# Optimization experiments

Measured on AMD Instinct MI355X. Metric: run time of the kernel, lower is better.

## Reference

```python
import jax, jax.numpy as jnp
import numpy as np

EMBED_DIM = 768
NUM_HEADS = 12
HEAD_DIM = EMBED_DIM // NUM_HEADS  # 64
SCALE = HEAD_DIM ** 0.5  # NOTE: source MULTIPLIES by sqrt(head_dim) (likely a bug, kept faithful)


def setup_inputs() -> dict:
    key = jax.random.key(0)
    kx, kq, kk, kv, ko = jax.random.split(key, 5)
    B, N, E = 8, 2048, EMBED_DIM
    s = 1.0 / np.sqrt(E)
    return {
        "x": jax.random.normal(kx, (B, N, E), dtype=jnp.float32),
        # nn.Linear weights stored [out_features, in_features], y = x @ W.T
        "Wq": jax.random.normal(kq, (E, E), dtype=jnp.float32) * s,
        "Wk": jax.random.normal(kk, (E, E), dtype=jnp.float32) * s,
        "Wv": jax.random.normal(kv, (E, E), dtype=jnp.float32) * s,
        "Wo": jax.random.normal(ko, (E, E), dtype=jnp.float32) * s,
    }


def reference(x, Wq, Wk, Wv, Wo):
    # Projections (no bias)
    q = jnp.einsum("bne,fe->bnf", x, Wq)
    k = jnp.einsum("bne,fe->bnf", x, Wk)
    v = jnp.einsum("bne,fe->bnf", x, Wv)
    # Full-width attention over the entire embedding dim (no head split, per source)
    energy = jnp.einsum("bid,bjd->bij", q, k) * SCALE  # [B, N, N]
    attn = jax.nn.softmax(energy, axis=-1)
    out = jnp.einsum("bij,bjd->bid", attn, v)  # [B, N, E]
    return jnp.einsum("bne,fe->bnf", out, Wo)
```

## Files before the change

kernel.cpp:

```cpp
#include <hip/hip_runtime.h>
#include <stdint.h>

typedef __bf16 bf16;
typedef __bf16 bf16x4 __attribute__((ext_vector_type(4)));
typedef __bf16 bf16x8 __attribute__((ext_vector_type(8)));
typedef float  f32x4  __attribute__((ext_vector_type(4)));

constexpr int BB = 8;
constexpr int NN = 2048;
constexpr int EE = 768;
constexpr int MM = BB * NN;

typedef const __attribute__((address_space(1))) void* as1_cvp;
typedef __attribute__((address_space(3))) void* as3_vp;

static __device__ __forceinline__ void gld16(const void* g, void* l) {
  __builtin_amdgcn_global_load_lds((as1_cvp)g, (as3_vp)l, 16, 0, 0);
}

__global__ __launch_bounds__(256) void k_splitx(const float4* __restrict__ x,
                                                bf16x4* __restrict__ hi,
                                                bf16x4* __restrict__ lo, int n4) {
  int i = blockIdx.x * 256 + threadIdx.x;
  int st = gridDim.x * 256;
  for (; i < n4; i += st) {
    float4 v = x[i];
    bf16x4 h, l;
    h[0] = (bf16)v.x; l[0] = (bf16)(v.x - (float)h[0]);
    h[1] = (bf16)v.y; l[1] = (bf16)(v.y - (float)h[1]);
    h[2] = (bf16)v.z; l[2] = (bf16)(v.z - (float)h[2]);
    h[3] = (bf16)v.w; l[3] = (bf16)(v.w - (float)h[3]);
    hi[i] = h; lo[i] = l;
  }
}

__global__ __launch_bounds__(256) void k_cvt(const float4* __restrict__ src,
                                             bf16x4* __restrict__ dst, int n4) {
  int i = blockIdx.x * 256 + threadIdx.x;
  int st = gridDim.x * 256;
  for (; i < n4; i += st) {
    float4 v = src[i];
    bf16x4 h;
    h[0] = (bf16)v.x; h[1] = (bf16)v.y; h[2] = (bf16)v.z; h[3] = (bf16)v.w;
    dst[i] = h;
  }
}

template <bool PAIR>
__global__ __launch_bounds__(256) void k_wtrans(const float* __restrict__ src,
                                                bf16* __restrict__ hi,
                                                bf16* __restrict__ lo) {
  __shared__ float t[64][65];
  int e0 = blockIdx.x * 64, f0 = blockIdx.y * 64;
  int tid = threadIdx.x;
#pragma unroll
  for (int h = 0; h < 4; h++) {
    int lin = h * 1024 + tid * 4;
    int r = lin >> 6, c = lin & 63;
    float4 v = *(const float4*)(src + (size_t)(f0 + r) * EE + e0 + c);
    t[r][c] = v.x; t[r][c + 1] = v.y; t[r][c + 2] = v.z; t[r][c + 3] = v.w;
  }
  __syncthreads();
#pragma unroll
  for (int h = 0; h < 4; h++) {
    int lin = h * 1024 + tid * 4;
    int er = lin >> 6, fc = lin & 63;
    bf16x4 oh, ol;
#pragma unroll
    for (int j = 0; j < 4; j++) {
      float v = t[fc + j][er];
      bf16 hh = (bf16)v;
      oh[j] = hh;
      if constexpr (PAIR) ol[j] = (bf16)(v - (float)hh);
    }
    *(bf16x4*)(hi + (size_t)(e0 + er) * EE + f0 + fc) = oh;
    if constexpr (PAIR) *(bf16x4*)(lo + (size_t)(e0 + er) * EE + f0 + fc) = ol;
  }
}

template <bool SPLIT, int EPI, int LB>
__global__ __launch_bounds__(256, LB) void k_gemm(
    const bf16* __restrict__ Ah, const bf16* __restrict__ Al,
    const bf16* __restrict__ Bh, const bf16* __restrict__ Bl,
    void* __restrict__ C0, void* __restrict__ C1,
    int Kdim, int lda, int ldb, int ldc,
    long long sA, long long sB, long long sC, float cscale) {
  constexpr int NTILES = SPLIT ? 4 : 2;
  __shared__ __align__(16) bf16 smm[NTILES * 128 * 64];
  bf16* smAh = smm;
  bf16* smBh = smm + 128 * 64;
  bf16* smAl = SPLIT ? smm + 2 * 128 * 64 : nullptr;
  bf16* smBl = SPLIT ? smm + 3 * 128 * 64 : nullptr;

  const int tid = threadIdx.x;
  const int lane = tid & 63, wid = tid >> 6;
  const int lr = lane & 15, lq = lane >> 4;
  const int wr = (wid >> 1) * 64, wc = (wid & 1) * 64;
  const long long bz = blockIdx.z;
  const int col0 = blockIdx.x * 128, row0 = blockIdx.y * 128;

  const bf16* pAh = Ah + bz * sA;
  const bf16* pBh = Bh + bz * sB;
  const bf16* pAl = SPLIT ? (Al + bz * sA) : nullptr;
  const bf16* pBl = SPLIT ? (Bl + bz * sB) : nullptr;

  f32x4 acc[4][4] = {};

  for (int kt = 0; kt < Kdim; kt += 64) {
    {
      int o = tid * 16;
#pragma unroll
      for (int r = 0; r < 4; r++, o += 4096) {
        int row = o >> 7;
        int c = (o & 127) ^ ((row & 7) << 4);
        gld16((const char*)(pAh + (size_t)(row0 + row) * lda + kt) + c, (char*)smAh + o);
        gld16((const char*)(pBh + (size_t)(col0 + row) * ldb + kt) + c, (char*)smBh + o);
        if constexpr (SPLIT) {
          gld16((const char*)(pAl + (size_t)(row0 + row) * lda + kt) + c, (char*)smAl + o);
          gld16((const char*)(pBl + (size_t)(col0 + row) * ldb + kt) + c, (char*)smBl + o);
        }
      }
    }
    __syncthreads();
#pragma unroll
    for (int kk = 0; kk < 2; kk++) {
      bf16x8 ah[4], bh[4], al[4], bl[4];
#pragma unroll
      for (int i = 0; i < 4; i++) {
        int ar = wr + i * 16 + lr;
        int ao = ar * 128 + ((kk * 64 + lq * 16) ^ ((ar & 7) << 4));
        ah[i] = *(const bf16x8*)((const char*)smAh + ao);
        int br = wc + i * 16 + lr;
        int bo = br * 128 + ((kk * 64 + lq * 16) ^ ((br & 7) << 4));
        bh[i] = *(const bf16x8*)((const char*)smBh + bo);
        if constexpr (SPLIT) {
          al[i] = *(const bf16x8*)((const char*)smAl + ao);
          bl[i] = *(const bf16x8*)((const char*)smBl + bo);
        }
      }
#pragma unroll
      for (int i = 0; i < 4; i++)
#pragma unroll
        for (int j = 0; j < 4; j++) {
          acc[i][j] = __builtin_amdgcn_mfma_f32_16x16x32_bf16(ah[i], bh[j], acc[i][j], 0, 0, 0);
          if constexpr (SPLIT) {
            acc[i][j] = __builtin_amdgcn_mfma_f32_16x16x32_bf16(ah[i], bl[j], acc[i][j], 0, 0, 0);
            acc[i][j] = __builtin_amdgcn_mfma_f32_16x16x32_bf16(al[i], bh[j], acc[i][j], 0, 0, 0);
          }
        }
    }
    __syncthreads();
  }

#pragma unroll
  for (int i = 0; i < 4; i++) {
#pragma unroll
    for (int j2 = 0; j2 < 4; j2++) {
      f32x4 v = acc[i][j2];
#pragma unroll
      for (int j = 0; j < 4; j++) {
        size_t r = (size_t)(row0 + wr + i * 16 + lq * 4 + j);
        size_t c = (size_t)(col0 + wc + j2 * 16 + lr);
        size_t idx = r * (size_t)ldc + c;
        float val = v[j] * cscale;
        if constexpr (EPI == 0) {
          bf16* Chp = (bf16*)C0 + bz * sC;
          bf16* Clp = (bf16*)C1 + bz * sC;
          bf16 h = (bf16)val;
          Chp[idx] = h;
          Clp[idx] = (bf16)(val - (float)h);
        } else if constexpr (EPI == 1) {
          float* Cp = (float*)C0 + bz * sC;
          Cp[idx] = val;
        } else {
          bf16* Cp = (bf16*)C0 + bz * sC;
          Cp[idx] = (bf16)val;
        }
      }
    }
  }
}

__global__ __launch_bounds__(256) void k_softmax(float* __restrict__ S) {
  size_t row = blockIdx.x;
  float* srow = S + row * (size_t)NN;
  int tid = threadIdx.x;
  int wid = tid >> 6, lane = tid & 63;
  const float4* s4 = (const float4*)srow;
  float4 v0 = s4[tid * 2], v1 = s4[tid * 2 + 1];
  float vv[8] = {v0.x, v0.y, v0.z, v0.w, v1.x, v1.y, v1.z, v1.w};
  float m = vv[0];
#pragma unroll
  for (int j = 1; j < 8; j++) m = fmaxf(m, vv[j]);
#pragma unroll
  for (int d = 1; d < 64; d <<= 1) m = fmaxf(m, __shfl_xor(m, d));
  __shared__ float red[8];
  if (lane == 0) red[wid] = m;
  __syncthreads();
  m = fmaxf(fmaxf(red[0], red[1]), fmaxf(red[2], red[3]));
  float e[8];
  float ssum = 0.f;
#pragma unroll
  for (int j = 0; j < 8; j++) { e[j] = __expf(vv[j] - m); ssum += e[j]; }
#pragma unroll
  for (int d = 1; d < 64; d <<= 1) ssum += __shfl_xor(ssum, d);
  if (lane == 0) red[4 + wid] = ssum;
  __syncthreads();
  ssum = red[4] + red[5] + red[6] + red[7];
  float inv = 1.0f / ssum;
  bf16x8 p;
#pragma unroll
  for (int j = 0; j < 8; j++) p[j] = (bf16)(e[j] * inv);
  *(bf16x8*)((bf16*)srow + tid * 8) = p;
}

extern "C" void kernel_launch(void* const* d_in, const int* in_sizes, int n_in,
                              void* d_out, int out_size, void* d_ws, size_t ws_size,
                              hipStream_t stream) {
  const float* x  = (const float*)d_in[0];
  const float* Wq = (const float*)d_in[1];
  const float* Wk = (const float*)d_in[2];
  const float* Wv = (const float*)d_in[3];
  const float* Wo = (const float*)d_in[4];
  float* out = (float*)d_out;
  char* ws = (char*)d_ws;

  const size_t szXE = (size_t)MM * EE * 2;
  const size_t szWb = (size_t)EE * EE * 2;
  const size_t szS1 = (size_t)NN * NN * 4;

  bf16* xhi = (bf16*)(ws);
  bf16* xlo = (bf16*)(ws + szXE);
  char* wb  = ws + 2 * szXE;
  bf16* wqTh = (bf16*)(wb);
  bf16* wqTl = (bf16*)(wb + 1 * szWb);
  bf16* wkTh = (bf16*)(wb + 2 * szWb);
  bf16* wkTl = (bf16*)(wb + 3 * szWb);
  bf16* wvT  = (bf16*)(wb + 4 * szWb);
  bf16* wob  = (bf16*)(wb + 5 * szWb);
  bf16* wqkTh = (bf16*)(wb + 6 * szWb);
  bf16* wqkTl = (bf16*)(wb + 7 * szWb);
  bf16* wvob  = (bf16*)(wb + 8 * szWb);
  char* yb = wb + 9 * szWb;
  bf16* Yh = (bf16*)(yb);
  bf16* Yl = (bf16*)(yb + szXE);
  bf16* Ut = (bf16*)(yb + 2 * szXE);
  char* Sb = yb + 3 * szXE;
  float* S = (float*)Sb;

  size_t oS = (size_t)(Sb - ws);
  size_t avail = ws_size > oS ? ws_size - oS : 0;
  int G = 8;
  while (G > 1 && (size_t)G * szS1 > avail) G >>= 1;

  k_splitx<<<2048, 256, 0, stream>>>((const float4*)x, (bf16x4*)xhi, (bf16x4*)xlo, MM * EE / 4);
  k_cvt<<<64, 256, 0, stream>>>((const float4*)Wo, (bf16x4*)wob, EE * EE / 4);
  k_wtrans<true><<<dim3(12, 12), 256, 0, stream>>>(Wq, wqTh, wqTl);
  k_wtrans<true><<<dim3(12, 12), 256, 0, stream>>>(Wk, wkTh, wkTl);
  k_wtrans<false><<<dim3(12, 12), 256, 0, stream>>>(Wv, wvT, nullptr);

  k_gemm<true, 0, 2><<<dim3(EE / 128, EE / 128, 1), 256, 0, stream>>>(
      wkTh, wkTl, wqTh, wqTl, wqkTh, wqkTl, EE, EE, EE, EE, 0, 0, 0, 1.0f);
  k_gemm<false, 2, 4><<<dim3(EE / 128, EE / 128, 1), 256, 0, stream>>>(
      wob, nullptr, wvT, nullptr, wvob, nullptr, EE, EE, EE, EE, 0, 0, 0, 1.0f);
  k_gemm<true, 0, 2><<<dim3(EE / 128, MM / 128, 1), 256, 0, stream>>>(
      xhi, xlo, wqkTh, wqkTl, Yh, Yl, EE, EE, EE, EE, 0, 0, 0, 1.0f);
  k_gemm<false, 2, 4><<<dim3(MM / 128, EE / 128, 1), 256, 0, stream>>>(
      wvob, nullptr, xhi, nullptr, Ut, nullptr, EE, EE, EE, MM, 0, 0, 0, 1.0f);

  const long long sNE = (long long)NN * EE;
  for (int g = 0; g < BB; g += G) {
    k_gemm<true, 1, 2><<<dim3(NN / 128, NN / 128, G), 256, 0, stream>>>(
        Yh + (size_t)g * sNE, Yl + (size_t)g * sNE,
        xhi + (size_t)g * sNE, xlo + (size_t)g * sNE,
        S, nullptr, EE, EE, EE, NN, sNE, sNE, (long long)NN * NN, 8.0f);
    k_softmax<<<G * NN, 256, 0, stream>>>(S);
    k_gemm<false, 1, 4><<<dim3(EE / 128, NN / 128, G), 256, 0, stream>>>(
        (const bf16*)S, nullptr, Ut + (size_t)g * NN, nullptr,
        out + (size_t)g * NN * EE, nullptr, NN, 2 * NN, MM, EE,
        2LL * NN * NN, (long long)NN, (long long)NN * EE, 1.0f);
  }
}
```

Before: 418.9 us.

## Load B-low fragments directly from global memory and fuse weight prep kernels

Merges the four weight conversion and transpose launches into one k_prep kernel, so fewer launches are needed. In the split-precision GEMMs it adds a BLDIR mode that reads the low-part B operand straight from global memory into registers instead of staging it in LDS. That cuts LDS from four tiles to three and raises the launch-bounds occupancy hint from 2 to 3. It also adds a SWAP option that transposes the block grid for the Y projection. The trade is uncoalesced, unpipelined global loads inside the MFMA loop, which may add latency.

Measured after the change: 443.5 us. 5.9% more time.

```diff
diff --git a/kernel.cpp b/kernel.cpp
--- a/kernel.cpp
+++ b/kernel.cpp
@@ -34,25 +34,34 @@
   }
 }
 
-__global__ __launch_bounds__(256) void k_cvt(const float4* __restrict__ src,
-                                             bf16x4* __restrict__ dst, int n4) {
-  int i = blockIdx.x * 256 + threadIdx.x;
-  int st = gridDim.x * 256;
-  for (; i < n4; i += st) {
-    float4 v = src[i];
-    bf16x4 h;
-    h[0] = (bf16)v.x; h[1] = (bf16)v.y; h[2] = (bf16)v.z; h[3] = (bf16)v.w;
-    dst[i] = h;
-  }
-}
-
-template <bool PAIR>
-__global__ __launch_bounds__(256) void k_wtrans(const float* __restrict__ src,
-                                                bf16* __restrict__ hi,
-                                                bf16* __restrict__ lo) {
+__global__ __launch_bounds__(256) void k_prep(const float* __restrict__ wq,
+                                              const float* __restrict__ wk,
+                                              const float* __restrict__ wv,
+                                              const float* __restrict__ wo,
+                                              bf16* __restrict__ qTh, bf16* __restrict__ qTl,
+                                              bf16* __restrict__ kTh, bf16* __restrict__ kTl,
+                                              bf16* __restrict__ vT,  bf16* __restrict__ ob) {
   __shared__ float t[64][65];
+  int z = blockIdx.z;
+  int tid = threadIdx.x;
+  if (z == 3) {
+    int blk = blockIdx.y * 12 + blockIdx.x;
+    const float4* s4 = (const float4*)wo;
+#pragma unroll
+    for (int j = 0; j < 4; j++) {
+      int i = blk * 1024 + j * 256 + tid;
+      float4 v = s4[i];
+      bf16x4 h;
+      h[0] = (bf16)v.x; h[1] = (bf16)v.y; h[2] = (bf16)v.z; h[3] = (bf16)v.w;
+      ((bf16x4*)ob)[i] = h;
+    }
+    return;
+  }
+  const float* src = z == 0 ? wq : (z == 1 ? wk : wv);
+  bf16* hi = z == 0 ? qTh : (z == 1 ? kTh : vT);
+  bf16* lo = z == 0 ? qTl : kTl;
+  bool pair = z < 2;
   int e0 = blockIdx.x * 64, f0 = blockIdx.y * 64;
-  int tid = threadIdx.x;
 #pragma unroll
   for (int h = 0; h < 4; h++) {
     int lin = h * 1024 + tid * 4;
@@ -71,38 +80,42 @@
       float v = t[fc + j][er];
       bf16 hh = (bf16)v;
       oh[j] = hh;
-      if constexpr (PAIR) ol[j] = (bf16)(v - (float)hh);
+      ol[j] = (bf16)(v - (float)hh);
     }
     *(bf16x4*)(hi + (size_t)(e0 + er) * EE + f0 + fc) = oh;
-    if constexpr (PAIR) *(bf16x4*)(lo + (size_t)(e0 + er) * EE + f0 + fc) = ol;
-  }
-}
-
-template <bool SPLIT, int EPI, int LB>
+    if (pair) *(bf16x4*)(lo + (size_t)(e0 + er) * EE + f0 + fc) = ol;
+  }
+}
+
+template <bool SPLIT, int EPI, int LB, bool SWAP, bool BLDIR>
 __global__ __launch_bounds__(256, LB) void k_gemm(
     const bf16* __restrict__ Ah, const bf16* __restrict__ Al,
     const bf16* __restrict__ Bh, const bf16* __restrict__ Bl,
     void* __restrict__ C0, void* __restrict__ C1,
     int Kdim, int lda, int ldb, int ldc,
     long long sA, long long sB, long long sC, float cscale) {
-  constexpr int NTILES = SPLIT ? 4 : 2;
+  constexpr int NTILES = SPLIT ? (BLDIR ? 3 : 4) : 2;
   __shared__ __align__(16) bf16 smm[NTILES * 128 * 64];
   bf16* smAh = smm;
-  bf16* smBh = smm + 128 * 64;
-  bf16* smAl = SPLIT ? smm + 2 * 128 * 64 : nullptr;
-  bf16* smBl = SPLIT ? smm + 3 * 128 * 64 : nullptr;
+  bf16* smBh = smm + 8192;
+  bf16* smAl = SPLIT ? smm + 16384 : nullptr;
+  bf16* smBl = (SPLIT && !BLDIR) ? smm + 24576 : nullptr;
 
   const int tid = threadIdx.x;
   const int lane = tid & 63, wid = tid >> 6;
   const int lr = lane & 15, lq = lane >> 4;
   const int wr = (wid >> 1) * 64, wc = (wid & 1) * 64;
   const long long bz = blockIdx.z;
-  const int col0 = blockIdx.x * 128, row0 = blockIdx.y * 128;
+  const int bx = SWAP ? blockIdx.y : blockIdx.x;
+  const int by = SWAP ? blockIdx.x : blockIdx.y;
+  const int col0 = bx * 128, row0 = by * 128;
 
   const bf16* pAh = Ah + bz * sA;
   const bf16* pBh = Bh + bz * sB;
   const bf16* pAl = SPLIT ? (Al + bz * sA) : nullptr;
   const bf16* pBl = SPLIT ? (Bl + bz * sB) : nullptr;
+  const bf16* blbase = (SPLIT && BLDIR)
+      ? (pBl + (size_t)(col0 + wc + lr) * ldb + lq * 8) : nullptr;
 
   f32x4 acc[4][4] = {};
 
@@ -117,7 +130,8 @@
         gld16((const char*)(pBh + (size_t)(col0 + row) * ldb + kt) + c, (char*)smBh + o);
         if constexpr (SPLIT) {
           gld16((const char*)(pAl + (size_t)(row0 + row) * lda + kt) + c, (char*)smAl + o);
-          gld16((const char*)(pBl + (size_t)(col0 + row) * ldb + kt) + c, (char*)smBl + o);
+          if constexpr (!BLDIR)
+            gld16((const char*)(pBl + (size_t)(col0 + row) * ldb + kt) + c, (char*)smBl + o);
         }
       }
     }
@@ -135,7 +149,10 @@
         bh[i] = *(const bf16x8*)((const char*)smBh + bo);
         if constexpr (SPLIT) {
           al[i] = *(const bf16x8*)((const char*)smAl + ao);
-          bl[i] = *(const bf16x8*)((const char*)smBl + bo);
+          if constexpr (BLDIR)
+            bl[i] = *(const bf16x8*)(blbase + (size_t)(i * 16) * ldb + kt + kk * 32);
+          else
+            bl[i] = *(const bf16x8*)((const char*)smBl + bo);
         }
       }
 #pragma unroll
@@ -254,28 +271,26 @@
   while (G > 1 && (size_t)G * szS1 > avail) G >>= 1;
 
   k_splitx<<<2048, 256, 0, stream>>>((const float4*)x, (bf16x4*)xhi, (bf16x4*)xlo, MM * EE / 4);
-  k_cvt<<<64, 256, 0, stream>>>((const float4*)Wo, (bf16x4*)wob, EE * EE / 4);
-  k_wtrans<true><<<dim3(12, 12), 256, 0, stream>>>(Wq, wqTh, wqTl);
-  k_wtrans<true><<<dim3(12, 12), 256, 0, stream>>>(Wk, wkTh, wkTl);
-  k_wtrans<false><<<dim3(12, 12), 256, 0, stream>>>(Wv, wvT, nullptr);
-
-  k_gemm<true, 0, 2><<<dim3(EE / 128, EE / 128, 1), 256, 0, stream>>>(
+  k_prep<<<dim3(12, 12, 4), 256, 0, stream>>>(Wq, Wk, Wv, Wo,
+                                              wqTh, wqTl, wkTh, wkTl, wvT, wob);
+
+  k_gemm<true, 0, 2, false, false><<<dim3(EE / 128, EE / 128, 1), 256, 0, stream>>>(
       wkTh, wkTl, wqTh, wqTl, wqkTh, wqkTl, EE, EE, EE, EE, 0, 0, 0, 1.0f);
-  k_gemm<false, 2, 4><<<dim3(EE / 128, EE / 128, 1), 256, 0, stream>>>(
+  k_gemm<false, 2, 4, false, false><<<dim3(EE / 128, EE / 128, 1), 256, 0, stream>>>(
       wob, nullptr, wvT, nullptr, wvob, nullptr, EE, EE, EE, EE, 0, 0, 0, 1.0f);
-  k_gemm<true, 0, 2><<<dim3(EE / 128, MM / 128, 1), 256, 0, stream>>>(
+  k_gemm<true, 0, 3, true, true><<<dim3(MM / 128, EE / 128, 1), 256, 0, stream>>>(
       xhi, xlo, wqkTh, wqkTl, Yh, Yl, EE, EE, EE, EE, 0, 0, 0, 1.0f);
-  k_gemm<false, 2, 4><<<dim3(MM / 128, EE / 128, 1), 256, 0, stream>>>(
+  k_gemm<false, 2, 4, false, false><<<dim3(MM / 128, EE / 128, 1), 256, 0, stream>>>(
       wvob, nullptr, xhi, nullptr, Ut, nullptr, EE, EE, EE, MM, 0, 0, 0, 1.0f);
 
   const long long sNE = (long long)NN * EE;
   for (int g = 0; g < BB; g += G) {
-    k_gemm<true, 1, 2><<<dim3(NN / 128, NN / 128, G), 256, 0, stream>>>(
+    k_gemm<true, 1, 3, false, true><<<dim3(NN / 128, NN / 128, G), 256, 0, stream>>>(
         Yh + (size_t)g * sNE, Yl + (size_t)g * sNE,
         xhi + (size_t)g * sNE, xlo + (size_t)g * sNE,
         S, nullptr, EE, EE, EE, NN, sNE, sNE, (long long)NN * NN, 8.0f);
     k_softmax<<<G * NN, 256, 0, stream>>>(S);
-    k_gemm<false, 1, 4><<<dim3(EE / 128, NN / 128, G), 256, 0, stream>>>(
+    k_gemm<false, 1, 4, false, false><<<dim3(EE / 128, NN / 128, G), 256, 0, stream>>>(
         (const bf16*)S, nullptr, Ut + (size_t)g * NN, nullptr,
         out + (size_t)g * NN * EE, nullptr, NN, 2 * NN, MM, EE,
         2LL * NN * NN, (long long)NN, (long long)NN * EE, 1.0f);
```
